# Optimization experiments

Measured on AMD Instinct MI355X. Metric: run time of the kernel, lower is better.

The kernel has to match this reference:

```python
import jax, jax.numpy as jnp
import numpy as np

H_FEAT, W_FEAT, K_ANCH = 512, 512, 9
FIELD = 32.0
IMG_W, IMG_H = int(W_FEAT * FIELD), int(H_FEAT * FIELD)
TOP_K = 4000          # pre-NMS candidate cap (fixed size for jit)
THRESHOLD = 0.5       # objectness threshold (call() default)
NMS_IOU = 0.3         # constructor default


def setup_inputs() -> dict:
    key = jax.random.key(0)
    k1, k2 = jax.random.split(key)
    output_obj = jax.random.normal(k1, (H_FEAT, W_FEAT, 2 * K_ANCH), jnp.float32)
    output_reg = jax.random.normal(k2, (H_FEAT, W_FEAT, 4 * K_ANCH), jnp.float32) * 0.05
    anchor_px = jnp.array([16, 32, 48, 64, 96, 128, 192, 256, 384], jnp.int32)
    # create_anchors: square anchors centered on each feature-map cell
    ys, xs = jnp.meshgrid(jnp.arange(H_FEAT, dtype=jnp.float32),
                          jnp.arange(W_FEAT, dtype=jnp.float32), indexing='ij')
    cx = (xs + 0.5) * FIELD            # [H, W]
    cy = (ys + 0.5) * FIELD
    w = anchor_px.astype(jnp.float32)  # [K]
    ax = cx[:, :, None] - w[None, None, :] / 2.0   # [H, W, K]
    ay = cy[:, :, None] - w[None, None, :] / 2.0
    aw = jnp.broadcast_to(w[None, None, :], (H_FEAT, W_FEAT, K_ANCH))
    anchors = jnp.stack([ax, ay, aw, aw], axis=-1).reshape(-1, 4)  # [H*W*K, 4]
    return {"output_obj": output_obj, "output_reg": output_reg,
            "anchors": anchors, "anchor_px": anchor_px}


def map_outputs(output, anchors, anchor_px):
    # vectorized version of per-anchor tf.map_fn(argmax) + gather_nd
    K = anchor_px.shape[0]
    idx = jnp.argmax(anchors[:, 3:4].astype(jnp.int32) == anchor_px[None, :], axis=1)
    px = ((anchors[:, 0] + anchors[:, 2] / 2.0) / FIELD).astype(jnp.int32)
    py = ((anchors[:, 1] + anchors[:, 3] / 2.0) / FIELD).astype(jnp.int32)
    D = output.shape[-1] // K
    reshaped = output.reshape(output.shape[0], output.shape[1], K, D)
    return reshaped[py, px, idx]   # [H*W*K, D]


def unparameterize(reg, anchors):
    cx = anchors[:, 0] + anchors[:, 2] / 2.0 + reg[:, 0] * anchors[:, 2]
    cy = anchors[:, 1] + anchors[:, 3] / 2.0 + reg[:, 1] * anchors[:, 3]
    w = anchors[:, 2] * jnp.exp(reg[:, 2])
    h = anchors[:, 3] * jnp.exp(reg[:, 3])
    return jnp.stack([cx - w / 2.0, cy - h / 2.0, w, h], axis=1)


def clip_boxes(boxes, width, height):
    x1 = jnp.clip(boxes[:, 0], 0.0, width)
    y1 = jnp.clip(boxes[:, 1], 0.0, height)
    x2 = jnp.clip(boxes[:, 0] + boxes[:, 2], 0.0, width)
    y2 = jnp.clip(boxes[:, 1] + boxes[:, 3], 0.0, height)
    return jnp.stack([x1, y1, x2 - x1, y2 - y1], axis=1)


def forward(output_obj, output_reg, anchors, anchor_px):
    rpn_obj = jax.nn.softmax(map_outputs(output_obj, anchors, anchor_px), axis=-1)
    rpn_reg = map_outputs(output_reg, anchors, anchor_px)
    rpn_boxes = clip_boxes(unparameterize(rpn_reg, anchors), float(IMG_W), float(IMG_H))
    scores = rpn_obj[:, 1]
    # threshold(): boolean_mask -> realized as score masking + fixed-size top-k
    masked = jnp.where(scores > THRESHOLD, scores, -1.0)
    top_scores, top_idx = jax.lax.top_k(masked, TOP_K)
    b = rpn_boxes[top_idx]        # [TOP_K, 4], sorted by score desc
    o = rpn_obj[top_idx]          # [TOP_K, 2]
    valid = top_scores > THRESHOLD
    # pairwise IoU in corner form
    x1, y1 = b[:, 0], b[:, 1]
    x2, y2 = x1 + b[:, 2], y1 + b[:, 3]
    area = b[:, 2] * b[:, 3]
    iw = jnp.clip(jnp.minimum(x2[:, None], x2[None, :]) - jnp.maximum(x1[:, None], x1[None, :]), 0.0)
    ih = jnp.clip(jnp.minimum(y2[:, None], y2[None, :]) - jnp.maximum(y1[:, None], y1[None, :]), 0.0)
    inter = iw * ih
    iou = inter / (area[:, None] + area[None, :] - inter + 1e-8)
    rng = jnp.arange(TOP_K)
    # greedy NMS over score-sorted candidates (tf.image.non_max_suppression)
    def body(i, keep):
        sup = (iou[i] > NMS_IOU) & (rng > i) & keep[i]
        return keep & jnp.logical_not(sup)
    keep = jax.lax.fori_loop(0, TOP_K, body, valid)
    return b, o, keep


def reference(output_obj, output_reg, anchors, anchor_px):
    return forward(output_obj, output_reg, anchors, anchor_px)
```

## Files before the change

### kernel.cpp

```cpp
#include <hip/hip_runtime.h>
#include <cstdint>
#include <math.h>

#pragma clang fp contract(off)

typedef unsigned int u32;
typedef unsigned long long u64;

#define HFEAT 512
#define WFEAT 512
#define NPIX (HFEAT*WFEAT)
#define NANCH (NPIX*9)
#define TOPK 4000
#define IMG_SZ 16384.0f
#define NBUCKET 8192
#define CAP 32768
#define NWORD 63
#define RCACHE 224
#define COARSE_CUT (-3.5f)
#define COARSE_BUK_SAFE 1537

#define WS_META 32768
#define WS_SUP  32832
#define WS_CKEY 33856
#define WS_NX1  312000
#define WS_NY1  328000
#define WS_NX2  344000
#define WS_NY2  360000
#define WS_NAR  376000
#define WS_VAL  392000
#define WS_MASK 408000
#define WS_RANK WS_MASK
#define WS_COARSE (WS_MASK + 524288)
#define WS_DIAG 2456000

__device__ __forceinline__ int dbucket_bits(u32 bits) {
    int b = (int)((bits - 0xC0000000u) >> 12);
    return (b > (NBUCKET - 1)) ? (NBUCKET - 1) : b;
}

__device__ __forceinline__ float score1(float d) {
    float e0 = (float)::exp((double)d);
    float den = e0 + 1.0f;
    return 1.0f / den;
}

__device__ __forceinline__ void softmax2(float l0, float l1, float& s0, float& s1) {
    float m = fmaxf(l0, l1);
    float a0 = l0 - m;
    float a1 = l1 - m;
    float e0 = (float)::exp((double)a0);
    float e1 = (float)::exp((double)a1);
    float den = e0 + e1;
    s0 = e0 / den;
    s1 = e1 / den;
}

__global__ void k_zero(u32* ws32) {
    int t = threadIdx.x;
    if (t < 144) ws32[WS_META/4 + t] = 0;
}

__global__ void k_coarse(const float4* __restrict__ o4, u64* __restrict__ coarse,
                         u32* __restrict__ meta) {
    __shared__ u64 stage[512];
    __shared__ u32 scnt, sbase;
    int tid = threadIdx.x;
    if (tid == 0) scnt = 0;
    __syncthreads();
    int base = blockIdx.x * 2304;
#pragma unroll
    for (int k = 0; k < 9; ++k) {
        int a4 = base + k * 256 + tid;
        float4 v = o4[a4];
        float d0 = v.x - v.y;
        float d1 = v.z - v.w;
        if (d0 < COARSE_CUT) {
            u32 p = atomicAdd(&scnt, 1u);
            if (p < 512) stage[p] = ((u64)__float_as_uint(d0) << 32) | (u32)(2*a4);
        }
        if (d1 < COARSE_CUT) {
            u32 p = atomicAdd(&scnt, 1u);
            if (p < 512) stage[p] = ((u64)__float_as_uint(d1) << 32) | (u32)(2*a4 + 1);
        }
    }
    __syncthreads();
    u32 cntr = scnt;
    u32 cnt = (cntr > 512u) ? 512u : cntr;
    if (tid == 0 && cntr) {
        sbase = atomicAdd(&meta[3], (cntr > 512u) ? (u32)CAP : cnt);
    }
    __syncthreads();
    if (cnt)
        for (u32 t = tid; t < cnt; t += 256) {
            u32 pos = sbase + t;
            if (pos < CAP) coarse[pos] = stage[t];
        }
}

__global__ __launch_bounds__(1024) void k_selectkey(const float* __restrict__ obj,
                                                    u32* __restrict__ meta,
                                                    const u64* __restrict__ coarse,
                                                    u64* __restrict__ ckeyp) {
    __shared__ u32 lh[NBUCKET];
    __shared__ u32 ss[1024];
    __shared__ u32 ps[1024];
    __shared__ u32 thr_s;
    int tid = threadIdx.x;
    for (int b = tid; b < NBUCKET; b += 1024) lh[b] = 0;
    if (tid == 0) thr_s = 0;
    __syncthreads();
    u32 coarseN = meta[3];
    bool ok = (coarseN >= (u32)TOPK) && (coarseN < (u32)CAP);
    if (ok) {
        for (u32 t = tid; t < coarseN; t += 1024)
            atomicAdd(&lh[dbucket_bits((u32)(coarse[t] >> 32))], 1u);
    }
    __syncthreads();
    u32 local = 0;
#pragma unroll
    for (int j = 0; j < 8; ++j) local += lh[tid*8 + j];
    ss[tid] = local;
    __syncthreads();
    for (int off = 1; off < 1024; off <<= 1) {
        u32 v = (tid + off < 1024) ? ss[tid + off] : 0;
        __syncthreads();
        ss[tid] += v;
        __syncthreads();
    }
    if (ok) {
        u32 S_t = ss[tid];
        u32 S_next = (tid < 1023) ? ss[tid+1] : 0;
        if (S_t >= TOPK && S_next < TOPK) {
            u32 cum = S_next;
            int bsel = tid*8;
            for (int b = tid*8 + 7; b >= tid*8; --b) {
                cum += lh[b];
                if (cum >= TOPK) { bsel = b; break; }
            }
            thr_s = (u32)((bsel > 0) ? bsel - 1 : 0);
        }
    }
    __syncthreads();
    bool fast = ok && (thr_s >= (u32)COARSE_BUK_SAFE);
    if (fast) {
        int thr = (int)thr_s;
        u32 mycnt = 0;
        for (u32 t = tid; t < coarseN; t += 1024)
            if (dbucket_bits((u32)(coarse[t] >> 32)) >= thr) mycnt++;
        ps[tid] = mycnt;
        __syncthreads();
        for (int off = 1; off < 1024; off <<= 1) {
            u32 v = (tid >= off) ? ps[tid - off] : 0;
            __syncthreads();
            ps[tid] += v;
            __syncthreads();
        }
        u32 w = ps[tid] - mycnt;
        for (u32 t = tid; t < coarseN; t += 1024) {
            u64 e = coarse[t];
            u32 dbits = (u32)(e >> 32);
            if (dbucket_bits(dbits) >= thr) {
                float s1 = score1(__uint_as_float(dbits));
                ckeyp[w++] = ((u64)__float_as_uint(s1) << 32) |
                             (u32)(~(u32)(e & 0xFFFFFFFFull));
            }
        }
        if (tid == 0) { meta[0] = ps[1023]; meta[1] = thr_s; meta[5] = 1u; }
    } else {
        const float2* o2 = (const float2*)obj;
        for (int a = tid; a < NANCH; a += 1024) {
            float2 v = o2[a];
            float d = v.x - v.y;
            if (d < 0.0f) {
                float s1 = score1(d);
                if (s1 > 0.5f) {
                    u32 pos = atomicAdd(&meta[0], 1u);
                    if (pos < CAP)
                        ckeyp[pos] = ((u64)__float_as_uint(s1) << 32) | (u32)(~(u32)a);
                }
            }
        }
        if (tid == 0) meta[5] = 0u;
    }
}

#define RSL 1024
#define NSLICE 4
__global__ void k_rank(const u32* __restrict__ meta, const u64* __restrict__ ckeyp,
                       u32* __restrict__ rankbuf) {
    __shared__ u64 lk[RSL];
    int tid = threadIdx.x;
    u32 Mu = meta[0];
    int M = (int)(Mu < (u32)CAP ? Mu : (u32)CAP);
    int c = blockIdx.y * 256 + tid;
    if (blockIdx.y * 256 >= M) return;
    bool act = (c < M);
    u64 mypk = act ? ckeyp[c] : 0ull;
    int cnt = 0;
    for (int t0 = blockIdx.x * RSL; t0 < M; t0 += NSLICE * RSL) {
        __syncthreads();
        for (int j = tid; j < RSL; j += 256)
            lk[j] = (t0 + j < M) ? ckeyp[t0 + j] : 0ull;
        __syncthreads();
#pragma unroll 16
        for (int j = 0; j < RSL; ++j)
            cnt += (lk[j] > mypk) ? 1 : 0;
    }
    rankbuf[blockIdx.x * CAP + c] = (u32)cnt;
}

__global__ void k_selgather(const u32* __restrict__ meta, const u64* __restrict__ ckeyp,
                            const u32* __restrict__ rankbuf,
                            const float* __restrict__ obj, const float* __restrict__ reg,
                            const float* __restrict__ anch, float* __restrict__ out,
                            float* __restrict__ nx1, float* __restrict__ ny1,
                            float* __restrict__ nx2, float* __restrict__ ny2,
                            float* __restrict__ nar, u32* __restrict__ valid) {
    u32 Mu = meta[0];
    int M = (int)(Mu < (u32)CAP ? Mu : (u32)CAP);
    int c = blockIdx.x * 256 + threadIdx.x;
    if (c >= M) return;
    u32 r = rankbuf[c] + rankbuf[CAP + c] + rankbuf[2*CAP + c] + rankbuf[3*CAP + c];
    if (r >= TOPK) return;
    u32 i = ~(u32)(ckeyp[c] & 0xFFFFFFFFull);
    u32 p = i / 9u, k = i - p * 9u;
    float l0 = obj[(size_t)p*18 + 2*k];
    float l1 = obj[(size_t)p*18 + 2*k + 1];
    float s0, s1;
    softmax2(l0, l1, s0, s1);
    const float* rg = reg + (size_t)p*36 + 4*k;
    float t0 = rg[0], t1 = rg[1], t2 = rg[2], t3 = rg[3];
    const float* an = anch + (size_t)i*4;
    float a0 = an[0], a1 = an[1], a2 = an[2], a3 = an[3];
    float cx = a0 + a2/2.0f + t0*a2;
    float cy = a1 + a3/2.0f + t1*a3;
    float w = a2 * (float)::exp((double)t2);
    float h = a3 * (float)::exp((double)t3);
    float bx = cx - w/2.0f;
    float by = cy - h/2.0f;
    float x1 = fminf(fmaxf(bx, 0.0f), IMG_SZ);
    float y1 = fminf(fmaxf(by, 0.0f), IMG_SZ);
    float x2 = fminf(fmaxf(bx + w, 0.0f), IMG_SZ);
    float y2 = fminf(fmaxf(by + h, 0.0f), IMG_SZ);
    float bw = x2 - x1, bh = y2 - y1;
    out[4*r+0] = x1;
    out[4*r+1] = y1;
    out[4*r+2] = bw;
    out[4*r+3] = bh;
    out[16000 + 2*r]     = s0;
    out[16000 + 2*r + 1] = s1;
    nx1[r] = x1; ny1[r] = y1;
    nx2[r] = x1 + bw;
    ny2[r] = y1 + bh;
    nar[r] = bw * bh;
    valid[r] = (s1 > 0.5f) ? 1u : 0u;
}

__device__ __forceinline__ bool iou_gt(float x1a, float y1a, float x2a, float y2a, float aA,
                                       float x1b, float y1b, float x2b, float y2b, float aB) {
    float iw = fminf(x2a, x2b) - fmaxf(x1a, x1b);
    float ih = fminf(y2a, y2b) - fmaxf(y1a, y1b);
    iw = fmaxf(iw, 0.0f);
    ih = fmaxf(ih, 0.0f);
    float inter = iw * ih;
    float iou = inter / (aA + aB - inter + 1e-8f);
    return iou > 0.3f;
}

__global__ void k_mask(const float* __restrict__ nx1, const float* __restrict__ ny1,
                       const float* __restrict__ nx2, const float* __restrict__ ny2,
                       const float* __restrict__ nar, u64* __restrict__ mask,
                       u64* __restrict__ diag, u64* __restrict__ supany) {
    __shared__ float cx1[64], cy1[64], cx2[64], cy2[64], car[64];
    int w = blockIdx.y;
    int j0 = w * 64;
    int tid = threadIdx.x;
    int i = blockIdx.x * 256 + tid;
    if (j0 + 63 < (int)(blockIdx.x * 256)) {
        if (i < TOPK) mask[(size_t)i * 64 + w] = 0ull;
        return;
    }
    if (tid < 64) {
        int j = j0 + tid;
        bool v = j < TOPK;
        cx1[tid] = v ? nx1[j] : 1e9f;
        cy1[tid] = v ? ny1[j] : 1e9f;
        cx2[tid] = v ? nx2[j] : 1e9f;
        cy2[tid] = v ? ny2[j] : 1e9f;
        car[tid] = v ? nar[j] : 0.f;
    }
    __syncthreads();
    if (i >= TOPK) return;
    float x1 = nx1[i], y1 = ny1[i], x2 = nx2[i], y2 = ny2[i], ar = nar[i];
    u64 bits = 0;
#pragma unroll
    for (int b = 0; b < 64; ++b) {
        int j = j0 + b;
        if (j < TOPK && j > i &&
            iou_gt(x1, y1, x2, y2, ar, cx1[b], cy1[b], cx2[b], cy2[b], car[b]))
            bits |= (1ull << b);
    }
    mask[(size_t)i * 64 + w] = bits;
    if (w == (i >> 6)) diag[i] = bits;
    u64 anyb = __ballot(bits != 0ull);
    if ((tid & 63) == 0 && anyb) atomicOr(&supany[i >> 6], anyb);
}

__global__ __launch_bounds__(512) void k_scan_nms(const u64* __restrict__ mask,
                                                  const u64* __restrict__ diag,
                                                  const u64* __restrict__ supany,
                                                  const u32* __restrict__ valid,
                                                  float* __restrict__ out) {
    __shared__ u64 dlds[NWORD * 64];
    __shared__ u64 cache[RCACHE * 64];
    __shared__ u32 rowlist[RCACHE];
    __shared__ u32 nrows_s;
    __shared__ u64 vml[64];
    __shared__ u64 keep_s[64];
    int tid = threadIdx.x;
    int wave = tid >> 6, lane = tid & 63;

    for (int g = wave; g < 64; g += 8) {
        int t = g * 64 + lane;
        u32 v = (t < TOPK) ? valid[t] : 0u;
        u64 bm = __ballot(v != 0u);
        if (lane == 0) vml[g] = bm;
    }
    for (int t = tid; t < NWORD * 64; t += 512)
        dlds[t] = (t < TOPK) ? diag[t] : 0ull;

    int excl = 0;
    u64 sa = 0;
    if (wave == 0) {
        sa = supany[lane];
        int c = (int)__popcll(sa);
        int pfx = c;
        for (int off = 1; off < 64; off <<= 1) {
            int n = __shfl_up(pfx, off);
            if (lane >= off) pfx += n;
        }
        excl = pfx - c;
        int total = __shfl(pfx, 63);
        if (lane == 0) nrows_s = (u32)((total < RCACHE) ? total : RCACHE);
        int s = excl; u64 t = sa;
        while (t) {
            int b = (int)__builtin_ctzll(t); t &= t - 1;
            if (s < RCACHE) rowlist[s] = (u32)((lane << 6) | b);
            s++;
        }
    }
    __syncthreads();
    int R = (int)nrows_s;
    {
        const int TW = RCACHE * 64;
        for (int t0 = tid; t0 < TW; t0 += 512 * 8) {
            u64 v[8];
#pragma unroll
            for (int u = 0; u < 8; ++u) {
                int t = t0 + u * 512;
                int sl = t >> 6;
                int row = (t < TW && sl < R) ? (int)rowlist[sl] : 0;
                v[u] = (t < TW) ? mask[(size_t)row * 64 + (t & 63)] : 0ull;
            }
#pragma unroll
            for (int u = 0; u < 8; ++u) {
                int t = t0 + u * 512;
                if (t < TW) cache[t] = v[u];
            }
        }
    }
    __syncthreads();
    if (wave == 0) {
        u64 kw = vml[lane];
        u64 gm = __ballot((sa & kw) != 0ull);
        while (gm) {
            int g = (int)__builtin_ctzll(gm); gm &= gm - 1;
            u64 wg  = __shfl(kw, g);
            u64 sag = __shfl(sa, g);
            u64 supAlive = wg & sag;
            if (supAlive == 0ull) continue;
            int sbase = __shfl(excl, g);
            u64 dg = dlds[(g << 6) | lane];
            u64 am = wg, act = supAlive, keptSup = 0ull;
            while (act) {
                int s = (int)__builtin_ctzll(act);
                u64 sup = __shfl(dg, s);
                am &= ~sup;
                keptSup |= (1ull << s);
                act &= ~(1ull << s);
                act &= am;
            }
            u64 acc = 0, t = keptSup;
            while (t) {
                int s1b = (int)__builtin_ctzll(t); t &= t - 1;
                int sl1 = sbase + (int)__popcll(sag & ((1ull << s1b) - 1ull));
                if (t) {
                    int s2b = (int)__builtin_ctzll(t); t &= t - 1;
                    int sl2 = sbase + (int)__popcll(sag & ((1ull << s2b) - 1ull));
                    u64 ra = (sl1 < RCACHE) ? cache[(sl1 << 6) | lane]
                                            : mask[(size_t)((g << 6) | s1b) * 64 + lane];
                    u64 rb = (sl2 < RCACHE) ? cache[(sl2 << 6) | lane]
                                            : mask[(size_t)((g << 6) | s2b) * 64 + lane];
                    acc |= ra | rb;
                } else {
                    acc |= (sl1 < RCACHE) ? cache[(sl1 << 6) | lane]
                                          : mask[(size_t)((g << 6) | s1b) * 64 + lane];
                }
            }
            kw &= ~acc;
        }
        keep_s[lane] = kw;
    }
    __syncthreads();
    for (int t = tid; t < TOPK; t += 512)
        out[24000 + t] = ((keep_s[t >> 6] >> (t & 63)) & 1ull) ? 1.0f : 0.0f;
}

extern "C" void kernel_launch(void* const* d_in, const int* in_sizes, int n_in,
                              void* d_out, int out_size, void* d_ws, size_t ws_size,
                              hipStream_t stream) {
    const float* obj  = (const float*)d_in[0];
    const float* reg  = (const float*)d_in[1];
    const float* anch = (const float*)d_in[2];
    float* out = (float*)d_out;
    char* ws = (char*)d_ws;

    u32* meta = (u32*)(ws + WS_META);
    u64* supany = (u64*)(ws + WS_SUP);
    u64* ckeyp = (u64*)(ws + WS_CKEY);
    float* nx1 = (float*)(ws + WS_NX1);
    float* ny1 = (float*)(ws + WS_NY1);
    float* nx2 = (float*)(ws + WS_NX2);
    float* ny2 = (float*)(ws + WS_NY2);
    float* nar = (float*)(ws + WS_NAR);
    u32* valid = (u32*)(ws + WS_VAL);
    u64* mask  = (u64*)(ws + WS_MASK);
    u64* diag  = (u64*)(ws + WS_DIAG);
    u32* rankbuf = (u32*)(ws + WS_RANK);
    u64* coarse  = (u64*)(ws + WS_COARSE);

    hipLaunchKernelGGL(k_zero, dim3(1), dim3(256), 0, stream, (u32*)ws);
    hipLaunchKernelGGL(k_coarse, dim3(NANCH / 4608), dim3(256), 0, stream,
                       (const float4*)obj, coarse, meta);
    hipLaunchKernelGGL(k_selectkey, dim3(1), dim3(1024), 0, stream, obj, meta, coarse, ckeyp);
    hipLaunchKernelGGL(k_rank, dim3(NSLICE, CAP/256), dim3(256), 0, stream, meta, ckeyp, rankbuf);
    hipLaunchKernelGGL(k_selgather, dim3(CAP/256), dim3(256), 0, stream,
                       meta, ckeyp, rankbuf, obj, reg, anch, out,
                       nx1, ny1, nx2, ny2, nar, valid);
    hipLaunchKernelGGL(k_mask, dim3((TOPK + 255) / 256, 64), dim3(256), 0, stream,
                       nx1, ny1, nx2, ny2, nar, mask, diag, supany);
    hipLaunchKernelGGL(k_scan_nms, dim3(1), dim3(512), 0, stream, mask, diag, supany, valid, out);
}
```

Baseline: 106.1 us.

## Split select-key into single-block threshold pass and grid-wide key compaction

The single-block select kernel, which both found the histogram threshold and compacted the surviving coarse candidates into keys, is split in two. A one-block kernel now only computes the threshold and fast-path flag into meta. A separate kernel launched with many blocks compacts candidates using block-local staging and one global atomic per block. The fallback full scan is also spread across that grid. This replaces a serial 1024-thread scan and compaction with wide parallelism, at the cost of one more launch and a key order that is no longer deterministic, which the later rank pass should tolerate.

```diff
diff --git a/kernel.cpp b/kernel.cpp
--- a/kernel.cpp
+++ b/kernel.cpp
@@ -98,17 +98,12 @@
         }
 }
 
-__global__ __launch_bounds__(1024) void k_selectkey(const float* __restrict__ obj,
-                                                    u32* __restrict__ meta,
-                                                    const u64* __restrict__ coarse,
-                                                    u64* __restrict__ ckeyp) {
+__global__ __launch_bounds__(1024) void k_select(const u64* __restrict__ coarse,
+                                                 u32* __restrict__ meta) {
     __shared__ u32 lh[NBUCKET];
     __shared__ u32 ss[1024];
-    __shared__ u32 ps[1024];
-    __shared__ u32 thr_s;
     int tid = threadIdx.x;
     for (int b = tid; b < NBUCKET; b += 1024) lh[b] = 0;
-    if (tid == 0) thr_s = 0;
     __syncthreads();
     u32 coarseN = meta[3];
     bool ok = (coarseN >= (u32)TOPK) && (coarseN < (u32)CAP);
@@ -128,60 +123,68 @@
         ss[tid] += v;
         __syncthreads();
     }
-    if (ok) {
-        u32 S_t = ss[tid];
-        u32 S_next = (tid < 1023) ? ss[tid+1] : 0;
-        if (S_t >= TOPK && S_next < TOPK) {
-            u32 cum = S_next;
-            int bsel = tid*8;
-            for (int b = tid*8 + 7; b >= tid*8; --b) {
-                cum += lh[b];
-                if (cum >= TOPK) { bsel = b; break; }
-            }
-            thr_s = (u32)((bsel > 0) ? bsel - 1 : 0);
-        }
-    }
-    __syncthreads();
-    bool fast = ok && (thr_s >= (u32)COARSE_BUK_SAFE);
+    if (!ok) { if (tid == 0) { meta[1] = 0; meta[5] = 0; } return; }
+    u32 S_t = ss[tid];
+    u32 S_next = (tid < 1023) ? ss[tid+1] : 0;
+    if (S_t >= TOPK && S_next < TOPK) {
+        u32 cum = S_next;
+        int bsel = tid*8;
+        for (int b = tid*8 + 7; b >= tid*8; --b) {
+            cum += lh[b];
+            if (cum >= TOPK) { bsel = b; break; }
+        }
+        u32 thr = (u32)((bsel > 0) ? bsel - 1 : 0);
+        meta[1] = thr;
+        meta[5] = (thr >= COARSE_BUK_SAFE) ? 1u : 0u;
+    }
+}
+
+__global__ void k_key(const float* __restrict__ obj, u32* __restrict__ meta,
+                      const u64* __restrict__ coarse, u64* __restrict__ ckeyp) {
+    __shared__ u64 stage[256];
+    __shared__ u32 scnt, sbase;
+    int tid = threadIdx.x;
+    if (tid == 0) scnt = 0;
+    __syncthreads();
+    bool fast = meta[5] != 0u;
     if (fast) {
-        int thr = (int)thr_s;
-        u32 mycnt = 0;
-        for (u32 t = tid; t < coarseN; t += 1024)
-            if (dbucket_bits((u32)(coarse[t] >> 32)) >= thr) mycnt++;
-        ps[tid] = mycnt;
-        __syncthreads();
-        for (int off = 1; off < 1024; off <<= 1) {
-            u32 v = (tid >= off) ? ps[tid - off] : 0;
+        u32 coarseN = meta[3];
+        int thr = (int)meta[1];
+        u32 t = blockIdx.x * 256 + tid;
+        if (blockIdx.x * 256 < coarseN) {
+            if (t < coarseN) {
+                u64 e = coarse[t];
+                u32 dbits = (u32)(e >> 32);
+                if (dbucket_bits(dbits) >= thr) {
+                    float s1 = score1(__uint_as_float(dbits));
+                    u32 bits = __float_as_uint(s1);
+                    u32 p = atomicAdd(&scnt, 1u);
+                    stage[p] = ((u64)bits << 32) | (u32)(~(u32)(e & 0xFFFFFFFFull));
+                }
+            }
             __syncthreads();
-            ps[tid] += v;
+            u32 cnt = scnt;
+            if (tid == 0 && cnt) sbase = atomicAdd(&meta[0], cnt);
             __syncthreads();
-        }
-        u32 w = ps[tid] - mycnt;
-        for (u32 t = tid; t < coarseN; t += 1024) {
-            u64 e = coarse[t];
-            u32 dbits = (u32)(e >> 32);
-            if (dbucket_bits(dbits) >= thr) {
-                float s1 = score1(__uint_as_float(dbits));
-                ckeyp[w++] = ((u64)__float_as_uint(s1) << 32) |
-                             (u32)(~(u32)(e & 0xFFFFFFFFull));
-            }
-        }
-        if (tid == 0) { meta[0] = ps[1023]; meta[1] = thr_s; meta[5] = 1u; }
+            if (cnt && tid < cnt) {
+                u32 pos = sbase + tid;
+                if (pos < CAP) ckeyp[pos] = stage[tid];
+            }
+        }
     } else {
         const float2* o2 = (const float2*)obj;
-        for (int a = tid; a < NANCH; a += 1024) {
+        for (int a = blockIdx.x * 256 + tid; a < NANCH; a += gridDim.x * 256) {
             float2 v = o2[a];
             float d = v.x - v.y;
             if (d < 0.0f) {
                 float s1 = score1(d);
                 if (s1 > 0.5f) {
+                    u32 bits = __float_as_uint(s1);
                     u32 pos = atomicAdd(&meta[0], 1u);
-                    if (pos < CAP)
-                        ckeyp[pos] = ((u64)__float_as_uint(s1) << 32) | (u32)(~(u32)a);
+                    if (pos < CAP) ckeyp[pos] = ((u64)bits << 32) | (u32)(~(u32)a);
                 }
             }
         }
-        if (tid == 0) meta[5] = 0u;
     }
 }
 
@@ -443,7 +446,8 @@
     hipLaunchKernelGGL(k_zero, dim3(1), dim3(256), 0, stream, (u32*)ws);
     hipLaunchKernelGGL(k_coarse, dim3(NANCH / 4608), dim3(256), 0, stream,
                        (const float4*)obj, coarse, meta);
-    hipLaunchKernelGGL(k_selectkey, dim3(1), dim3(1024), 0, stream, obj, meta, coarse, ckeyp);
+    hipLaunchKernelGGL(k_select, dim3(1), dim3(1024), 0, stream, coarse, meta);
+    hipLaunchKernelGGL(k_key, dim3(CAP/256), dim3(256), 0, stream, obj, meta, coarse, ckeyp);
     hipLaunchKernelGGL(k_rank, dim3(NSLICE, CAP/256), dim3(256), 0, stream, meta, ckeyp, rankbuf);
     hipLaunchKernelGGL(k_selgather, dim3(CAP/256), dim3(256), 0, stream,
                        meta, ckeyp, rankbuf, obj, reg, anch, out,
```

After: 97.78 us. -7.9%, faster.
